# Optimization experiments

Hardware: AMD Instinct MI355X
Metric: run time of the kernel (lower is better)

The kernel has to match this reference:

```python
import jax, jax.numpy as jnp
import numpy as np

POOLED_SIZES = [12, 16, 20, 24]
NUM_HEADS = 8
EPS_LN = 1e-5


def _pool_mat(in_size, out_size):
    # torch adaptive_avg_pool1d/2d semantics as an averaging matrix [out, in]
    m = np.zeros((out_size, in_size), np.float32)
    for i in range(out_size):
        s = (i * in_size) // out_size
        e = -((-(i + 1) * in_size) // out_size)  # ceil
        m[i, s:e] = 1.0 / (e - s)
    return jnp.asarray(m)


def _dwconv(x, w, b):
    # depthwise 3x3, stride 1, padding 1 (NCHW, OIHW with I=1)
    y = jax.lax.conv_general_dilated(
        x, w, (1, 1), 'SAME', feature_group_count=x.shape[1],
        dimension_numbers=('NCHW', 'OIHW', 'NCHW'))
    return y + b[None, :, None, None]


def _ln(x, g, b):
    m = x.mean(-1, keepdims=True)
    v = jnp.mean((x - m) ** 2, axis=-1, keepdims=True)
    return (x - m) / jnp.sqrt(v + EPS_LN) * g + b


def setup_inputs() -> dict:
    key = jax.random.key(0)
    ks = jax.random.split(key, 16)
    B, H, W, C = 4, 56, 56, 256
    hid = 4 * C
    nrm = lambda k, shape, s=0.02: jax.random.normal(k, shape, jnp.float32) * s
    inp = {
        'x': jax.random.normal(ks[0], (B, H * W, C), jnp.float32),
        'cpe_w': nrm(ks[1], (C, 1, 3, 3)), 'cpe_b': jnp.zeros((C,), jnp.float32),
        'norm1_w': jnp.ones((C,), jnp.float32), 'norm1_b': jnp.zeros((C,), jnp.float32),
        'q_w': nrm(ks[2], (C, C)),
        'kv_w': nrm(ks[3], (2 * C, C)),
        'attn_norm_w': jnp.ones((C,), jnp.float32), 'attn_norm_b': jnp.zeros((C,), jnp.float32),
        'proj_w': nrm(ks[4], (C, C)), 'proj_b': jnp.zeros((C,), jnp.float32),
        'norm2_w': jnp.ones((C,), jnp.float32), 'norm2_b': jnp.zeros((C,), jnp.float32),
        'fc1_w': nrm(ks[5], (hid, C)), 'fc1_b': jnp.zeros((hid,), jnp.float32),
        'irb_conv_w': nrm(ks[6], (hid, 1, 3, 3)), 'irb_conv_b': jnp.zeros((hid,), jnp.float32),
        'fc2_w': nrm(ks[7], (C, hid)), 'fc2_b': jnp.zeros((C,), jnp.float32),
        'H': H, 'W': W,
    }
    for i in range(4):
        inp[f'dconv{i}_w'] = nrm(ks[8 + i], (C, 1, 3, 3))
        inp[f'dconv{i}_b'] = jnp.zeros((C,), jnp.float32)
    return inp


def _forward(x, cpe_w, cpe_b, norm1_w, norm1_b, q_w, kv_w, attn_norm_w, attn_norm_b,
             proj_w, proj_b, dconv0_w, dconv0_b, dconv1_w, dconv1_b, dconv2_w, dconv2_b,
             dconv3_w, dconv3_b, norm2_w, norm2_b, fc1_w, fc1_b, irb_conv_w, irb_conv_b,
             fc2_w, fc2_b, H, W):
    B, N, C = x.shape
    nh = NUM_HEADS
    hd = C // nh
    scale = hd ** -0.5
    # conditional positional encoding: x = cpe(x) + x
    xi = x.transpose(0, 2, 1).reshape(B, C, H, W)
    xi = _dwconv(xi, cpe_w, cpe_b) + xi
    x = xi.reshape(B, C, N).transpose(0, 2, 1)
    # ---- pyramid pooling attention ----
    xn = _ln(x, norm1_w, norm1_b)
    q = (xn @ q_w.T).reshape(B, N, nh, hd).transpose(0, 2, 1, 3)  # [B,nh,N,hd]
    x_ = xn.transpose(0, 2, 1).reshape(B, C, H, W)
    dws = [(dconv0_w, dconv0_b), (dconv1_w, dconv1_b),
           (dconv2_w, dconv2_b), (dconv3_w, dconv3_b)]
    pools = []
    for p, (dw, db) in zip(POOLED_SIZES, dws):
        ph = _pool_mat(H, p)
        pw = _pool_mat(W, p)
        pool = jnp.einsum('oi,bcij,pj->bcop', ph, x_, pw)  # adaptive avg pool (p,p)
        pool = pool + _dwconv(pool, dw, db)
        pools.append(pool.reshape(B, C, -1))
    pools = jnp.concatenate(pools, axis=2).transpose(0, 2, 1)  # [B,P,C], P=1376
    pools = _ln(pools, attn_norm_w, attn_norm_b)
    kv = (pools @ kv_w.T).reshape(B, -1, 2, nh, hd).transpose(2, 0, 3, 1, 4)
    k, v = kv[0], kv[1]  # [B,nh,P,hd]
    attn = jax.nn.softmax(jnp.einsum('bhnd,bhpd->bhnp', q, k) * scale, axis=-1)
    out = jnp.einsum('bhnp,bhpd->bhnd', attn, v).transpose(0, 2, 1, 3).reshape(B, N, C)
    out = out @ proj_w.T + proj_b
    x = x + out
    # ---- IRB FFN ----
    xn = _ln(x, norm2_w, norm2_b)
    xi = xn.transpose(0, 2, 1).reshape(B, C, H, W)
    h = jnp.einsum('oc,bchw->bohw', fc1_w, xi) + fc1_b[None, :, None, None]
    h = jax.nn.gelu(h, approximate=False)
    h = h + _dwconv(h, irb_conv_w, irb_conv_b)
    o = jnp.einsum('oc,bchw->bohw', fc2_w, h) + fc2_b[None, :, None, None]
    x = x + o.reshape(B, C, N).transpose(0, 2, 1)
    return x


def reference(x, cpe_w, cpe_b, norm1_w, norm1_b, q_w, kv_w, attn_norm_w, attn_norm_b,
              proj_w, proj_b, dconv0_w, dconv0_b, dconv1_w, dconv1_b, dconv2_w, dconv2_b,
              dconv3_w, dconv3_b, norm2_w, norm2_b, fc1_w, fc1_b, irb_conv_w, irb_conv_b,
              fc2_w, fc2_b, H, W):
    return _forward(x, cpe_w, cpe_b, norm1_w, norm1_b, q_w, kv_w, attn_norm_w, attn_norm_b,
                    proj_w, proj_b, dconv0_w, dconv0_b, dconv1_w, dconv1_b, dconv2_w, dconv2_b,
                    dconv3_w, dconv3_b, norm2_w, norm2_b, fc1_w, fc1_b, irb_conv_w, irb_conv_b,
                    fc2_w, fc2_b, H, W)
```

## Files before the change

kernel.cpp:

```cpp
#include <hip/hip_runtime.h>
#include <hip/hip_bf16.h>

#define BQ 4
#define HH 56
#define WW 56
#define NN (HH*WW)
#define CC 256
#define NHEAD 8
#define HD 32
#define PP 1376
#define PPAD 1408
#define HIDN 1024
#define EPS_LN 1e-5f
#define QSCALE_LOG2E 0.25503484f

typedef unsigned short bf16u;
typedef __attribute__((ext_vector_type(8))) short short8;
typedef __attribute__((ext_vector_type(4))) float f32x4;

__device__ __forceinline__ float bf2f(bf16u u){
  union { unsigned int i; float f; } v; v.i = ((unsigned int)u) << 16; return v.f;
}
__device__ __forceinline__ bf16u f2bf(float f){
  unsigned int x = __float_as_uint(f);
  x += 0x7fffu + ((x >> 16) & 1u);
  return (bf16u)(x >> 16);
}
__device__ __forceinline__ bf16u f2bf_r(float f){
  return (bf16u)((__float_as_uint(f) + 0x8000u) >> 16);
}
__device__ __forceinline__ void cvt4(const ushort4 u, float* d){
  d[0]=bf2f(u.x); d[1]=bf2f(u.y); d[2]=bf2f(u.z); d[3]=bf2f(u.w);
}

__device__ __forceinline__ void bar_lgkm(){
  asm volatile("s_waitcnt lgkmcnt(0)" ::: "memory");
  __builtin_amdgcn_s_barrier();
  asm volatile("" ::: "memory");
}

#define CSEG 4
__global__ void k_init(const float* __restrict__ qw, const float* __restrict__ kvw,
                       const float* __restrict__ pw, const float* __restrict__ f1,
                       const float* __restrict__ f2, bf16u* __restrict__ wo,
                       const float* __restrict__ x, const float* __restrict__ w,
                       const float* __restrict__ bias, const float* __restrict__ g,
                       const float* __restrict__ be, float* __restrict__ x1,
                       bf16u* __restrict__ xnb){
  if (blockIdx.x < 768){
    int off = (blockIdx.x*256 + threadIdx.x) * 4;
    const float* s;
    if (off < 65536)       s = qw  + off;
    else if (off < 196608) s = kvw + off - 65536;
    else if (off < 262144) s = pw  + off - 196608;
    else if (off < 524288) s = f1  + off - 262144;
    else                   s = f2  + off - 524288;
    float4 v = *(const float4*)s;
    ushort4 u = {f2bf(v.x), f2bf(v.y), f2bf(v.z), f2bf(v.w)};
    *(ushort4*)(wo + off) = u;
    return;
  }
  int t = threadIdx.x;
  int wave = t >> 6, lane = t & 63;
  int widx = (blockIdx.x - 768)*4 + wave;
  const int nseg = WW/CSEG;
  int xseg = widx % nseg;
  int y    = (widx / nseg) % HH;
  int b    = widx / (nseg*HH);
  int c0 = lane*4;
  int x0 = xseg*CSEG;
  float wv[36];
  {
    const float* wp = w + (size_t)c0*9;
#pragma unroll
    for (int i = 0; i < 9; i++){
      float4 v = *(const float4*)(wp + i*4);
      wv[i*4+0]=v.x; wv[i*4+1]=v.y; wv[i*4+2]=v.z; wv[i*4+3]=v.w;
    }
  }
  float4 bi4 = *(const float4*)&bias[c0];
  float bi[4] = {bi4.x, bi4.y, bi4.z, bi4.w};
  float4 gv = *(const float4*)&g[c0];
  float4 bv = *(const float4*)&be[c0];
  const float* rowc = x + ((size_t)b*NN + (size_t)y*WW)*CC + c0;
  const float* rowm = (y > 0)    ? rowc - (size_t)WW*CC : rowc;
  const float* rowp = (y < HH-1) ? rowc + (size_t)WW*CC : rowc;
  if (y == 0){
#pragma unroll
    for (int cc = 0; cc < 4; cc++){ wv[cc*9+0]=0.f; wv[cc*9+1]=0.f; wv[cc*9+2]=0.f; }
  }
  if (y == HH-1){
#pragma unroll
    for (int cc = 0; cc < 4; cc++){ wv[cc*9+6]=0.f; wv[cc*9+7]=0.f; wv[cc*9+8]=0.f; }
  }
  float win[3][3][4];
  float4 rawA[3], rawB[3];
  if (x0 == 0){
#pragma unroll
    for (int r = 0; r < 3; r++)
#pragma unroll
      for (int cc = 0; cc < 4; cc++) win[0][r][cc] = 0.f;
  } else {
    size_t o = (size_t)(x0-1)*CC;
    float4 a0 = *(const float4*)&rowm[o];
    float4 a1 = *(const float4*)&rowc[o];
    float4 a2 = *(const float4*)&rowp[o];
    win[0][0][0]=a0.x; win[0][0][1]=a0.y; win[0][0][2]=a0.z; win[0][0][3]=a0.w;
    win[0][1][0]=a1.x; win[0][1][1]=a1.y; win[0][1][2]=a1.z; win[0][1][3]=a1.w;
    win[0][2][0]=a2.x; win[0][2][1]=a2.y; win[0][2][2]=a2.z; win[0][2][3]=a2.w;
  }
  {
    size_t o = (size_t)x0*CC;
    float4 a0 = *(const float4*)&rowm[o];
    float4 a1 = *(const float4*)&rowc[o];
    float4 a2 = *(const float4*)&rowp[o];
    win[1][0][0]=a0.x; win[1][0][1]=a0.y; win[1][0][2]=a0.z; win[1][0][3]=a0.w;
    win[1][1][0]=a1.x; win[1][1][1]=a1.y; win[1][1][2]=a1.z; win[1][1][3]=a1.w;
    win[1][2][0]=a2.x; win[1][2][1]=a2.y; win[1][2][2]=a2.z; win[1][2][3]=a2.w;
  }
  {
    size_t o = (size_t)(x0+1)*CC;
    rawA[0] = *(const float4*)&rowm[o];
    rawA[1] = *(const float4*)&rowc[o];
    rawA[2] = *(const float4*)&rowp[o];
  }
#pragma unroll
  for (int xx = 0; xx < CSEG; xx++){
    float4* cur = (xx & 1) ? rawB : rawA;
    float4* nxt = (xx & 1) ? rawA : rawB;
    if (xx < CSEG-1){
      int xg = x0 + xx + 2;
      if (xg < WW){
        size_t o = (size_t)xg*CC;
        nxt[0] = *(const float4*)&rowm[o];
        nxt[1] = *(const float4*)&rowc[o];
        nxt[2] = *(const float4*)&rowp[o];
      } else {
        float4 z = {0.f,0.f,0.f,0.f};
        nxt[0] = z; nxt[1] = z; nxt[2] = z;
      }
    }
    int sl2 = (xx+2)%3, slm = xx%3, slc = (xx+1)%3;
#pragma unroll
    for (int r = 0; r < 3; r++){
      win[sl2][r][0]=cur[r].x; win[sl2][r][1]=cur[r].y;
      win[sl2][r][2]=cur[r].z; win[sl2][r][3]=cur[r].w;
    }
    float o4[4];
#pragma unroll
    for (int cc = 0; cc < 4; cc++){
      float a = bi[cc];
      a += win[slm][0][cc]*wv[cc*9+0] + win[slc][0][cc]*wv[cc*9+1] + win[sl2][0][cc]*wv[cc*9+2];
      a += win[slm][1][cc]*wv[cc*9+3] + win[slc][1][cc]*wv[cc*9+4] + win[sl2][1][cc]*wv[cc*9+5];
      a += win[slm][2][cc]*wv[cc*9+6] + win[slc][2][cc]*wv[cc*9+7] + win[sl2][2][cc]*wv[cc*9+8];
      o4[cc] = win[slc][1][cc] + a;
    }
    size_t pix = (size_t)b*NN + (size_t)y*WW + x0 + xx;
    float4 ov = {o4[0],o4[1],o4[2],o4[3]};
    *(float4*)&x1[pix*CC + c0] = ov;
    float s  = o4[0]+o4[1]+o4[2]+o4[3];
    float s2 = o4[0]*o4[0]+o4[1]*o4[1]+o4[2]*o4[2]+o4[3]*o4[3];
#pragma unroll
    for (int off = 32; off; off >>= 1){
      s  += __shfl_xor(s,  off);
      s2 += __shfl_xor(s2, off);
    }
    float mean = s * (1.f/CC);
    float var  = s2 * (1.f/CC) - mean*mean;
    float rstd = rsqrtf(var + EPS_LN);
    float y0 = (o4[0]-mean)*rstd*gv.x + bv.x;
    float y1 = (o4[1]-mean)*rstd*gv.y + bv.y;
    float y2 = (o4[2]-mean)*rstd*gv.z + bv.z;
    float y3 = (o4[3]-mean)*rstd*gv.w + bv.w;
    ushort4 yb = {f2bf_r(y0), f2bf_r(y1), f2bf_r(y2), f2bf_r(y3)};
    *(ushort4*)&xnb[pix*CC + c0] = yb;
  }
}

__global__ void k_ln_bf16(const float* __restrict__ X, const float* __restrict__ g,
                          const float* __restrict__ be, bf16u* __restrict__ Y){
  int wave = threadIdx.x >> 6, lane = threadIdx.x & 63;
  int row = blockIdx.x*4 + wave;
  int c0 = lane*4;
  float4 v = *(const float4*)&X[(size_t)row*CC + c0];
  float s  = v.x+v.y+v.z+v.w;
  float s2 = v.x*v.x+v.y*v.y+v.z*v.z+v.w*v.w;
#pragma unroll
  for (int off = 32; off; off >>= 1){
    s  += __shfl_xor(s,  off);
    s2 += __shfl_xor(s2, off);
  }
  float mean = s * (1.f/CC);
  float var  = s2 * (1.f/CC) - mean*mean;
  float rstd = rsqrtf(var + EPS_LN);
  float4 gv = *(const float4*)&g[c0];
  float4 bv = *(const float4*)&be[c0];
  ushort4 yb = {f2bf_r((v.x-mean)*rstd*gv.x + bv.x),
                f2bf_r((v.y-mean)*rstd*gv.y + bv.y),
                f2bf_r((v.z-mean)*rstd*gv.z + bv.z),
                f2bf_r((v.w-mean)*rstd*gv.w + bv.w)};
  *(ushort4*)&Y[(size_t)row*CC + c0] = yb;
}

#define GST 40
template<int MT, int NT, bool OUT_BF16, bool HAS_BIAS, bool DO_GELU, bool HAS_RES, bool VT_OUT>
__device__ __forceinline__ void gemm_body(int bx, int by,
                       const bf16u* __restrict__ A, const bf16u* __restrict__ Wt,
                       const float* __restrict__ bias, void* Outp,
                       const float* Res, bf16u* __restrict__ vtout,
                       int Nout, int K, float oscale,
                       bf16u* __restrict__ AshB, bf16u* __restrict__ BshB){
  constexpr int MW = (MT == 128) ? 4 : 2;
  constexpr int NW = (NT == 128) ? 4 : 2;
  bf16u* Ash0 = AshB; bf16u* Ash1 = AshB + MT*GST;
  bf16u* Bsh0 = BshB; bf16u* Bsh1 = BshB + NT*GST;
  int t = threadIdx.x;
  int wave = t >> 6, lane = t & 63, quad = lane >> 4, l16 = lane & 15;
  int m0 = by * MT, n0 = bx * NT;
  int wm = (wave >> 1) * (MT/2);
  int wn = (wave & 1) * (NT/2);
  int ar = (MT==128) ? (t>>1) : (t>>2);
  int ac = (MT==128) ? ((t&1)*16) : ((t&3)*8);
  int br = (NT==128) ? (t>>1) : (t>>2);
  int bc = (NT==128) ? ((t&1)*16) : ((t&3)*8);
  int astore = ar*GST + ac;
  int bstore = br*GST + bc;
  const bf16u* ap = A  + (size_t)(m0+ar)*K + ac;
  const bf16u* bp = Wt + (size_t)(n0+br)*K + bc;

  {
    uint4 t0 = *(const uint4*)ap;
    *(uint4*)&Ash0[astore] = t0;
    if constexpr (MT == 128){ uint4 t1 = *(const uint4*)(ap+8); *(uint4*)&Ash0[astore+8] = t1; }
    uint4 t2 = *(const uint4*)bp;
    *(uint4*)&Bsh0[bstore] = t2;
    if constexpr (NT == 128){ uint4 t3 = *(const uint4*)(bp+8); *(uint4*)&Bsh0[bstore+8] = t3; }
  }
  uint4 aA0, aA1, bA0, bA1;
  uint4 aB0, aB1, bB0, bB1;
  ap += 32; bp += 32;
  aA0 = *(const uint4*)ap;
  if constexpr (MT == 128) aA1 = *(const uint4*)(ap+8);
  bA0 = *(const uint4*)bp;
  if constexpr (NT == 128) bA1 = *(const uint4*)(bp+8);
  ap += 32; bp += 32;
  aB0 = *(const uint4*)ap;
  if constexpr (MT == 128) aB1 = *(const uint4*)(ap+8);
  bB0 = *(const uint4*)bp;
  if constexpr (NT == 128) bB1 = *(const uint4*)(bp+8);
  ap += 32; bp += 32;
  bar_lgkm();

  f32x4 zero = {0.f,0.f,0.f,0.f};
  f32x4 acc[MW][NW];
#pragma unroll
  for (int i = 0; i < MW; i++)
#pragma unroll
    for (int j = 0; j < NW; j++) acc[i][j] = zero;

  int nks = K >> 5;

#define GEMM_STEP(AshP, BshP) { \
    short8 af[MW], bfr[NW]; \
    _Pragma("unroll") \
    for (int mi = 0; mi < MW; mi++) \
      af[mi] = *(const short8*)&AshP[(wm + mi*16 + l16)*GST + quad*8]; \
    _Pragma("unroll") \
    for (int ni = 0; ni < NW; ni++) \
      bfr[ni] = *(const short8*)&BshP[(wn + ni*16 + l16)*GST + quad*8]; \
    _Pragma("unroll") \
    for (int mi = 0; mi < MW; mi++) \
      _Pragma("unroll") \
      for (int ni = 0; ni < NW; ni++) \
        acc[mi][ni] = __builtin_amdgcn_mfma_f32_16x16x32_bf16(af[mi], bfr[ni], acc[mi][ni], 0,0,0); }

  for (int ks = 0; ks < nks; ks += 2){
    if (ks < nks-1){
      *(uint4*)&Ash1[astore] = aA0;
      if constexpr (MT == 128) *(uint4*)&Ash1[astore+8] = aA1;
      *(uint4*)&Bsh1[bstore] = bA0;
      if constexpr (NT == 128) *(uint4*)&Bsh1[bstore+8] = bA1;
      if (ks < nks-3){
        aA0 = *(const uint4*)ap;
        if constexpr (MT == 128) aA1 = *(const uint4*)(ap+8);
        bA0 = *(const uint4*)bp;
        if constexpr (NT == 128) bA1 = *(const uint4*)(bp+8);
        ap += 32; bp += 32;
      }
    }
    GEMM_STEP(Ash0, Bsh0)
    if (ks < nks-1) bar_lgkm();
    if (ks+1 < nks-1){
      *(uint4*)&Ash0[astore] = aB0;
      if constexpr (MT == 128) *(uint4*)&Ash0[astore+8] = aB1;
      *(uint4*)&Bsh0[bstore] = bB0;
      if constexpr (NT == 128) *(uint4*)&Bsh0[bstore+8] = bB1;
      if (ks+1 < nks-3){
        aB0 = *(const uint4*)ap;
        if constexpr (MT == 128) aB1 = *(const uint4*)(ap+8);
        bB0 = *(const uint4*)bp;
        if constexpr (NT == 128) bB1 = *(const uint4*)(bp+8);
        ap += 32; bp += 32;
      }
    }
    if (ks+1 < nks){
      GEMM_STEP(Ash1, Bsh1)
      if (ks+1 < nks-1) bar_lgkm();
    }
  }
#undef GEMM_STEP

#pragma unroll
  for (int mi = 0; mi < MW; mi++){
#pragma unroll
    for (int r = 0; r < 4; r++){
      int row = m0 + wm + mi*16 + quad*4 + r;
#pragma unroll
      for (int ni = 0; ni < NW; ni++){
        int col = n0 + wn + ni*16 + l16;
        float v = acc[mi][ni][r] * oscale;
        if constexpr (HAS_BIAS) v += bias[col];
        if constexpr (DO_GELU)  v = 0.5f*v*(1.f + erff(v*0.70710678118654752f));
        if constexpr (HAS_RES)  v += Res[(size_t)row*Nout + col];
        if constexpr (VT_OUT){
          if (col < CC){
            ((bf16u*)Outp)[(size_t)row*Nout + col] = f2bf_r(v);
          } else {
            int bb = row / PP, pp = row - bb*PP;
            vtout[((size_t)(bb*CC + (col - CC)))*PPAD + pp] = f2bf_r(v);
          }
        } else if constexpr (OUT_BF16){
          ((bf16u*)Outp)[(size_t)row*Nout + col] = f2bf_r(v);
        } else {
          ((float*)Outp)[(size_t)row*Nout + col] = v;
        }
      }
    }
  }
}

template<int MT, int NT, bool OUT_BF16, bool HAS_BIAS, bool DO_GELU, bool HAS_RES, bool VT_OUT>
__global__ __launch_bounds__(256) void k_gemm_mfma(const bf16u* __restrict__ A,
                       const bf16u* __restrict__ Wt,
                       const float* __restrict__ bias, void* Outp,
                       const float* Res, bf16u* __restrict__ vtout,
                       int NX, int Nout, int K, float oscale){
  __shared__ bf16u Ash[2][MT*GST];
  __shared__ bf16u Bsh[2][NT*GST];
  int i = blockIdx.x;
  int w = (i & 7) * ((int)gridDim.x >> 3) + (i >> 3);
  int bx = w % NX, by = w / NX;
  gemm_body<MT,NT,OUT_BF16,HAS_BIAS,DO_GELU,HAS_RES,VT_OUT>(
      bx, by, A, Wt, bias, Outp, Res, vtout, Nout, K, oscale,
      &Ash[0][0], &Bsh[0][0]);
}

#define QGRID ((CC/64)*(BQ*NN/64))
__global__ __launch_bounds__(256) void k_qpool(const bf16u* __restrict__ xnb,
                       const bf16u* __restrict__ wq, bf16u* __restrict__ qb,
                       float* __restrict__ praw){
  __shared__ bf16u Ash[2][64*GST];
  __shared__ bf16u Bsh[2][64*GST];
  if (blockIdx.x < QGRID){
    int i = blockIdx.x;
    int w = (i & 7) * (QGRID >> 3) + (i >> 3);
    int bx = w & 3, by = w >> 2;
    gemm_body<64,64,true,false,false,false,false>(
        bx, by, xnb, wq, nullptr, qb, nullptr, nullptr, CC, CC, QSCALE_LOG2E,
        &Ash[0][0], &Bsh[0][0]);
    return;
  }
  int wave = threadIdx.x >> 6, lane = threadIdx.x & 63;
  int bp = (blockIdx.x - QGRID)*4 + wave;
  int b = bp / PP, p = bp % PP;
  int ps, pi;
  if (p < 144)      { ps = 12; pi = p; }
  else if (p < 400) { ps = 16; pi = p - 144; }
  else if (p < 800) { ps = 20; pi = p - 400; }
  else              { ps = 24; pi = p - 800; }
  int oi = pi / ps, oj = pi % ps;
  int si = oi*HH/ps, ei = ((oi+1)*HH + ps - 1)/ps;
  int sj = oj*WW/ps, ej = ((oj+1)*WW + ps - 1)/ps;
  int c0 = lane*4;
  const bf16u* xb = xnb + (size_t)b*NN*CC + c0;
  float a0=0.f, a1=0.f, a2=0.f, a3=0.f;
  for (int i = si; i < ei; i++)
    for (int j = sj; j < ej; j++){
      ushort4 v = *(const ushort4*)&xb[(size_t)(i*WW+j)*CC];
      a0 += bf2f(v.x); a1 += bf2f(v.y); a2 += bf2f(v.z); a3 += bf2f(v.w);
    }
  float inv = 1.f / (float)((ei-si)*(ej-sj));
  float4 o = {a0*inv, a1*inv, a2*inv, a3*inv};
  *(float4*)&praw[(size_t)bp*CC + c0] = o;
}

__global__ void k_pooldw_ln(const float* __restrict__ praw,
    const float* w0, const float* b0, const float* w1, const float* b1,
    const float* w2, const float* b2, const float* w3, const float* b3,
    const float* __restrict__ g, const float* __restrict__ be,
    bf16u* __restrict__ pools){
  int bp = blockIdx.x;
  int b = bp / PP, p = bp % PP;
  int ps, pi, off; const float *w, *bi;
  if (p < 144)      { ps=12; pi=p;     off=0;   w=w0; bi=b0; }
  else if (p < 400) { ps=16; pi=p-144; off=144; w=w1; bi=b1; }
  else if (p < 800) { ps=20; pi=p-400; off=400; w=w2; bi=b2; }
  else              { ps=24; pi=p-800; off=800; w=w3; bi=b3; }
  int oi = pi/ps, oj = pi%ps;
  int c = threadIdx.x;
  const float* base = praw + (size_t)(b*PP + off)*CC + c;
  float acc = bi[c];
#pragma unroll
  for (int kh = 0; kh < 3; kh++){
    int ii = oi + kh - 1; if (ii < 0 || ii >= ps) continue;
#pragma unroll
    for (int kw = 0; kw < 3; kw++){
      int jj = oj + kw - 1; if (jj < 0 || jj >= ps) continue;
      acc += base[(size_t)(ii*ps+jj)*CC] * w[c*9 + kh*3 + kw];
    }
  }
  float v = base[(size_t)(oi*ps+oj)*CC] + acc;
  float s = v, s2 = v*v;
#pragma unroll
  for (int o2_ = 32; o2_; o2_ >>= 1){
    s  += __shfl_down(s,  o2_);
    s2 += __shfl_down(s2, o2_);
  }
  __shared__ float red[10];
  int wv_ = c >> 6, ln = c & 63;
  if (ln == 0){ red[wv_] = s; red[4+wv_] = s2; }
  __syncthreads();
  if (c == 0){
    float S  = red[0]+red[1]+red[2]+red[3];
    float S2 = red[4]+red[5]+red[6]+red[7];
    float mean = S * (1.f/CC);
    float var  = S2 * (1.f/CC) - mean*mean;
    red[8] = mean; red[9] = rsqrtf(var + EPS_LN);
  }
  __syncthreads();
  float mean = red[8], rstd = red[9];
  pools[(size_t)bp*CC + c] = f2bf_r((v - mean) * rstd * g[c] + be[c]);
}

#define KST 40
#define VST 72
__global__ __launch_bounds__(256) void k_attn_mfma(const bf16u* __restrict__ q,
                       const bf16u* __restrict__ kvb, const bf16u* __restrict__ vt,
                       bf16u* __restrict__ out){
  __shared__ bf16u Ksh[2][64*KST];
  __shared__ bf16u Vsh[2][32*VST];
  int t = threadIdx.x;
  int wave = t >> 6, lane = t & 63, quad = lane >> 4, l16 = lane & 15;
  int i = blockIdx.x;
  int bid = (i & 7) * 196 + (i >> 3);
  int qt = bid % (NN/64);
  int h  = (bid / (NN/64)) % NHEAD;
  int b  = bid / ((NN/64)*NHEAD);
  int q0 = qt*64 + wave*16;
  const bf16u* qptr = q + (size_t)(b*NN + q0 + l16)*CC + h*HD + quad*8;
  short8 qf = *(const short8*)qptr;
  f32x4 zero = {0.f,0.f,0.f,0.f};
  f32x4 o0 = zero, o1 = zero, osum = zero;
  const short8 onesf = {0x3F80,0x3F80,0x3F80,0x3F80,0x3F80,0x3F80,0x3F80,0x3F80};
  int ksr = t >> 2, ksc = (t & 3) * 8;
  int vsr = t >> 3, vsc = (t & 7) * 8;
  const bf16u* ksrc = kvb + (size_t)(b*PP + ksr)*(2*CC) + h*HD + ksc;
  const bf16u* vsrc = vt  + (size_t)(b*CC + h*HD + vsr)*PPAD + vsc;
  int krow = (ksr & 32) | ((ksr & 4) << 2) | ((ksr & 24) >> 1) | (ksr & 3);
  int kstore = krow*KST + ksc;
  int vstore = vsr*VST + vsc;
  int koffA = l16*KST + quad*8;
  int koffB = koffA + 16*KST;
  int voff0 = l16*VST + quad*8;
  int voff1 = (16 + l16)*VST + quad*8;

  uint4 kreg = *(const uint4*)ksrc;
  uint4 vreg = *(const uint4*)vsrc;
  *(uint4*)&Ksh[0][kstore] = kreg;
  *(uint4*)&Vsh[0][vstore] = vreg;
  ksrc += (size_t)64*(2*CC); vsrc += 64;
  kreg = *(const uint4*)ksrc; vreg = *(const uint4*)vsrc;
  bar_lgkm();

#define PAIR(KB, VB, cb) { \
    short8 kfa = *(const short8*)&KB[cb*KST + koffA]; \
    short8 kfb = *(const short8*)&KB[cb*KST + koffB]; \
    f32x4 sa = __builtin_amdgcn_mfma_f32_16x16x32_bf16(kfa, qf, zero, 0,0,0); \
    f32x4 sb = __builtin_amdgcn_mfma_f32_16x16x32_bf16(kfb, qf, zero, 0,0,0); \
    float ea0 = __builtin_amdgcn_exp2f(sa[0]), ea1 = __builtin_amdgcn_exp2f(sa[1]); \
    float ea2 = __builtin_amdgcn_exp2f(sa[2]), ea3 = __builtin_amdgcn_exp2f(sa[3]); \
    float eb0 = __builtin_amdgcn_exp2f(sb[0]), eb1 = __builtin_amdgcn_exp2f(sb[1]); \
    float eb2 = __builtin_amdgcn_exp2f(sb[2]), eb3 = __builtin_amdgcn_exp2f(sb[3]); \
    unsigned ra0 = __float_as_uint(ea0) + 0x8000u, ra1 = __float_as_uint(ea1) + 0x8000u; \
    unsigned ra2 = __float_as_uint(ea2) + 0x8000u, ra3 = __float_as_uint(ea3) + 0x8000u; \
    unsigned rb0 = __float_as_uint(eb0) + 0x8000u, rb1 = __float_as_uint(eb1) + 0x8000u; \
    unsigned rb2 = __float_as_uint(eb2) + 0x8000u, rb3 = __float_as_uint(eb3) + 0x8000u; \
    union { uint4 u; short8 s; } pk; \
    pk.u.x = __builtin_amdgcn_perm(ra1, ra0, 0x07060302u); \
    pk.u.y = __builtin_amdgcn_perm(ra3, ra2, 0x07060302u); \
    pk.u.z = __builtin_amdgcn_perm(rb1, rb0, 0x07060302u); \
    pk.u.w = __builtin_amdgcn_perm(rb3, rb2, 0x07060302u); \
    short8 pa = pk.s; \
    short8 vf0 = *(const short8*)&VB[cb + voff0]; \
    short8 vf1 = *(const short8*)&VB[cb + voff1]; \
    o0 = __builtin_amdgcn_mfma_f32_16x16x32_bf16(pa, vf0, o0, 0,0,0); \
    o1 = __builtin_amdgcn_mfma_f32_16x16x32_bf16(pa, vf1, o1, 0,0,0); \
    osum = __builtin_amdgcn_mfma_f32_16x16x32_bf16(pa, onesf, osum, 0,0,0); }

  for (int ch = 0; ch < PPAD/64 - 1; ch++){
    int cur = ch & 1;
    bf16u* KB = &Ksh[cur][0];
    bf16u* VB = &Vsh[cur][0];
    *(uint4*)&Ksh[cur^1][kstore] = kreg;
    *(uint4*)&Vsh[cur^1][vstore] = vreg;
    if (ch < PPAD/64 - 2){
      ksrc += (size_t)64*(2*CC); vsrc += 64;
      kreg = *(const uint4*)ksrc; vreg = *(const uint4*)vsrc;
    }
    PAIR(KB, VB, 0)
    PAIR(KB, VB, 32)
    bar_lgkm();
  }
  {
    bf16u* KB = &Ksh[1][0];
    bf16u* VB = &Vsh[1][0];
    PAIR(KB, VB, 0)
  }
#undef PAIR

#pragma unroll
  for (int r = 0; r < 4; r++){
    int qq = quad*4 + r;
    float inv = 1.f / osum[r];
    size_t base = (size_t)(b*NN + q0 + qq)*CC + h*HD;
    out[base + l16]      = f2bf_r(o0[r]*inv);
    out[base + 16 + l16] = f2bf_r(o1[r]*inv);
  }
}

#define DWSEG 8
__global__ __launch_bounds__(256) void k_dwh(const bf16u* __restrict__ h, const float* __restrict__ w,
                      const float* __restrict__ bias, bf16u* __restrict__ h2){
  const int nseg = WW/DWSEG;
  int bid = blockIdx.x;
  int xseg = bid % nseg;
  int y    = (bid / nseg) % HH;
  int b    = bid / (nseg*HH);
  int t = threadIdx.x;
  int c0 = t*4;
  int x0 = xseg*DWSEG;
  float wv[36];
  {
    const float4* wp = (const float4*)(w + (size_t)c0*9);
#pragma unroll
    for (int i = 0; i < 9; i++){
      float4 v = wp[i];
      wv[i*4+0]=v.x; wv[i*4+1]=v.y; wv[i*4+2]=v.z; wv[i*4+3]=v.w;
    }
  }
  float4 bi4 = *(const float4*)&bias[c0];
  float bi[4] = {bi4.x, bi4.y, bi4.z, bi4.w};
  const bf16u* rowc = h + ((size_t)b*NN + (size_t)y*WW)*HIDN + c0;
  const bf16u* rowm = (y > 0)    ? rowc - (size_t)WW*HIDN : rowc;
  const bf16u* rowp = (y < HH-1) ? rowc + (size_t)WW*HIDN : rowc;
  if (y == 0){
#pragma unroll
    for (int cc = 0; cc < 4; cc++){ wv[cc*9+0]=0.f; wv[cc*9+1]=0.f; wv[cc*9+2]=0.f; }
  }
  if (y == HH-1){
#pragma unroll
    for (int cc = 0; cc < 4; cc++){ wv[cc*9+6]=0.f; wv[cc*9+7]=0.f; wv[cc*9+8]=0.f; }
  }
  float win[3][3][4];
  ushort4 rawA[3], rawB[3];
  if (x0 == 0){
#pragma unroll
    for (int r = 0; r < 3; r++)
#pragma unroll
      for (int cc = 0; cc < 4; cc++) win[0][r][cc] = 0.f;
  } else {
    size_t o = (size_t)(x0-1)*HIDN;
    ushort4 a0 = *(const ushort4*)&rowm[o];
    ushort4 a1 = *(const ushort4*)&rowc[o];
    ushort4 a2 = *(const ushort4*)&rowp[o];
    cvt4(a0, win[0][0]); cvt4(a1, win[0][1]); cvt4(a2, win[0][2]);
  }
  {
    size_t o = (size_t)x0*HIDN;
    ushort4 a0 = *(const ushort4*)&rowm[o];
    ushort4 a1 = *(const ushort4*)&rowc[o];
    ushort4 a2 = *(const ushort4*)&rowp[o];
    cvt4(a0, win[1][0]); cvt4(a1, win[1][1]); cvt4(a2, win[1][2]);
  }
  {
    size_t o = (size_t)(x0+1)*HIDN;
    rawA[0] = *(const ushort4*)&rowm[o];
    rawA[1] = *(const ushort4*)&rowc[o];
    rawA[2] = *(const ushort4*)&rowp[o];
  }
#pragma unroll
  for (int x = 0; x < DWSEG; x++){
    ushort4* cur = (x & 1) ? rawB : rawA;
    ushort4* nxt = (x & 1) ? rawA : rawB;
    if (x < DWSEG-1){
      int xg = x0 + x + 2;
      if (xg < WW){
        size_t o = (size_t)xg*HIDN;
        nxt[0] = *(const ushort4*)&rowm[o];
        nxt[1] = *(const ushort4*)&rowc[o];
        nxt[2] = *(const ushort4*)&rowp[o];
      } else {
        ushort4 z = {0,0,0,0};
        nxt[0] = z; nxt[1] = z; nxt[2] = z;
      }
    }
    int s2 = (x+2)%3, sm = x%3, sc_ = (x+1)%3;
    cvt4(cur[0], win[s2][0]); cvt4(cur[1], win[s2][1]); cvt4(cur[2], win[s2][2]);
    float o0[4];
#pragma unroll
    for (int cc = 0; cc < 4; cc++){
      float a = bi[cc];
      a += win[sm][0][cc]*wv[cc*9+0] + win[sc_][0][cc]*wv[cc*9+1] + win[s2][0][cc]*wv[cc*9+2];
      a += win[sm][1][cc]*wv[cc*9+3] + win[sc_][1][cc]*wv[cc*9+4] + win[s2][1][cc]*wv[cc*9+5];
      a += win[sm][2][cc]*wv[cc*9+6] + win[sc_][2][cc]*wv[cc*9+7] + win[s2][2][cc]*wv[cc*9+8];
      o0[cc] = win[sc_][1][cc] + a;
    }
    ushort4 ou = {f2bf_r(o0[0]), f2bf_r(o0[1]), f2bf_r(o0[2]), f2bf_r(o0[3])};
    *(ushort4*)&h2[((size_t)b*NN + (size_t)y*WW + x0 + x)*HIDN + c0] = ou;
  }
}

extern "C" void kernel_launch(void* const* d_in, const int* in_sizes, int n_in,
                              void* d_out, int out_size, void* d_ws, size_t ws_size,
                              hipStream_t stream){
  const float* x      = (const float*)d_in[0];
  const float* cpe_w  = (const float*)d_in[1];
  const float* cpe_b  = (const float*)d_in[2];
  const float* n1w    = (const float*)d_in[3];
  const float* n1b    = (const float*)d_in[4];
  const float* q_w    = (const float*)d_in[5];
  const float* kv_w   = (const float*)d_in[6];
  const float* anw    = (const float*)d_in[7];
  const float* anb    = (const float*)d_in[8];
  const float* proj_w = (const float*)d_in[9];
  const float* proj_b = (const float*)d_in[10];
  const float* n2w    = (const float*)d_in[11];
  const float* n2b    = (const float*)d_in[12];
  const float* fc1_w  = (const float*)d_in[13];
  const float* fc1_b  = (const float*)d_in[14];
  const float* irb_w  = (const float*)d_in[15];
  const float* irb_b  = (const float*)d_in[16];
  const float* fc2_w  = (const float*)d_in[17];
  const float* fc2_b  = (const float*)d_in[18];
  const float* dw0    = (const float*)d_in[21];
  const float* db0    = (const float*)d_in[22];
  const float* dw1    = (const float*)d_in[23];
  const float* db1    = (const float*)d_in[24];
  const float* dw2    = (const float*)d_in[25];
  const float* db2    = (const float*)d_in[26];
  const float* dw3    = (const float*)d_in[27];
  const float* db3    = (const float*)d_in[28];

  const size_t BNC = (size_t)BQ*NN*CC;
  const size_t BPC = (size_t)BQ*PP*CC;
  const size_t BNH = (size_t)BQ*NN*HIDN;

  float* x1   = (float*)d_ws;
  bf16u* xnb  = (bf16u*)(x1 + BNC);
  bf16u* wbuf = xnb + BNC;
  bf16u* wq   = wbuf;
  bf16u* wkv  = wbuf + 65536;
  bf16u* wpj  = wbuf + 196608;
  bf16u* wf1  = wbuf + 262144;
  bf16u* wf2  = wbuf + 524288;
  float* A0   = (float*)(wbuf + 786432);
  bf16u* qb   = (bf16u*)A0;
  float* praw = (float*)(qb + BNC);
  bf16u* poolsb = (bf16u*)(praw + BPC);
  bf16u* kvb  = poolsb + BPC;
  bf16u* vtb  = kvb + (size_t)BQ*PP*2*CC;
  bf16u* hbuf = (bf16u*)A0;
  bf16u* h2buf = hbuf + BNH;

  k_init<<<768 + (BQ*HH*(WW/CSEG))/4, 256, 0, stream>>>(q_w, kv_w, proj_w, fc1_w, fc2_w, wbuf,
                                            x, cpe_w, cpe_b, n1w, n1b, x1, xnb);
  k_qpool<<<QGRID + BQ*PP/4, 256, 0, stream>>>(xnb, wq, qb, praw);
  k_pooldw_ln<<<BQ*PP, 256, 0, stream>>>(praw, dw0,db0, dw1,db1, dw2,db2, dw3,db3,
                                         anw, anb, poolsb);
  k_gemm_mfma<64,64,true,false,false,false,true><<<(2*CC/64)*(BQ*PP/64), 256, 0, stream>>>(
      poolsb, wkv, nullptr, kvb, nullptr, vtb, 2*CC/64, 2*CC, CC, 1.0f);
  k_attn_mfma<<<BQ*NHEAD*(NN/64), 256, 0, stream>>>(qb, kvb, vtb, qb);
  k_gemm_mfma<64,64,false,true,false,true,false><<<(CC/64)*(BQ*NN/64), 256, 0, stream>>>(
      qb, wpj, proj_b, x1, x1, nullptr, CC/64, CC, CC, 1.0f);
  k_ln_bf16<<<BQ*NN/4, 256, 0, stream>>>(x1, n2w, n2b, xnb);
  k_gemm_mfma<128,128,true,true,true,false,false><<<(HIDN/128)*(BQ*NN/128), 256, 0, stream>>>(
      xnb, wf1, fc1_b, hbuf, nullptr, nullptr, HIDN/128, HIDN, CC, 1.0f);
  k_dwh<<<BQ*HH*(WW/DWSEG), 256, 0, stream>>>(hbuf, irb_w, irb_b, h2buf);
  k_gemm_mfma<64,64,false,true,false,true,false><<<(CC/64)*(BQ*NN/64), 256, 0, stream>>>(
      h2buf, wf2, fc2_b, d_out, x1, nullptr, CC/64, CC, HIDN, 1.0f);
}
```

Baseline: 296.2 us.

## Deepen attention K/V prefetch to two chunks and shrink fc1 GEMM tile

The attention kernel's K/V streaming loop is unrolled by two with explicit ping-pong shared buffers. Global loads now run two chunks ahead using two register sets, so memory latency has more time to hide behind the MFMA and exp work. Separately, the fc1 GEMM tile changes from 128x128 to 64x128, doubling the block count for better occupancy and load balance. The cost is more live registers in attention and less data reuse per fc1 block.

```diff
diff --git a/kernel.cpp b/kernel.cpp
--- a/kernel.cpp
+++ b/kernel.cpp
@@ -466,6 +466,7 @@
   int vsr = t >> 3, vsc = (t & 7) * 8;
   const bf16u* ksrc = kvb + (size_t)(b*PP + ksr)*(2*CC) + h*HD + ksc;
   const bf16u* vsrc = vt  + (size_t)(b*CC + h*HD + vsr)*PPAD + vsc;
+  const size_t KSTEP = (size_t)64*(2*CC);
   int krow = (ksr & 32) | ((ksr & 4) << 2) | ((ksr & 24) >> 1) | (ksr & 3);
   int kstore = krow*KST + ksc;
   int vstore = vsr*VST + vsc;
@@ -473,18 +474,26 @@
   int koffB = koffA + 16*KST;
   int voff0 = l16*VST + quad*8;
   int voff1 = (16 + l16)*VST + quad*8;
-
-  uint4 kreg = *(const uint4*)ksrc;
-  uint4 vreg = *(const uint4*)vsrc;
-  *(uint4*)&Ksh[0][kstore] = kreg;
-  *(uint4*)&Vsh[0][vstore] = vreg;
-  ksrc += (size_t)64*(2*CC); vsrc += 64;
-  kreg = *(const uint4*)ksrc; vreg = *(const uint4*)vsrc;
+  bf16u* Ksh0 = &Ksh[0][0]; bf16u* Ksh1 = &Ksh[1][0];
+  bf16u* Vsh0 = &Vsh[0][0]; bf16u* Vsh1 = &Vsh[1][0];
+
+  {
+    uint4 k0 = *(const uint4*)ksrc;
+    uint4 v0 = *(const uint4*)vsrc;
+    *(uint4*)&Ksh0[kstore] = k0;
+    *(uint4*)&Vsh0[vstore] = v0;
+  }
+  uint4 kA, vA, kB, vB;
+  ksrc += KSTEP; vsrc += 64;
+  kA = *(const uint4*)ksrc; vA = *(const uint4*)vsrc;
+  ksrc += KSTEP; vsrc += 64;
+  kB = *(const uint4*)ksrc; vB = *(const uint4*)vsrc;
+  ksrc += KSTEP; vsrc += 64;
   bar_lgkm();
 
-#define PAIR(KB, VB, cb) { \
-    short8 kfa = *(const short8*)&KB[cb*KST + koffA]; \
-    short8 kfb = *(const short8*)&KB[cb*KST + koffB]; \
+#define PAIR(KB_, VB_, cb) { \
+    short8 kfa = *(const short8*)&KB_[cb*KST + koffA]; \
+    short8 kfb = *(const short8*)&KB_[cb*KST + koffB]; \
     f32x4 sa = __builtin_amdgcn_mfma_f32_16x16x32_bf16(kfa, qf, zero, 0,0,0); \
     f32x4 sb = __builtin_amdgcn_mfma_f32_16x16x32_bf16(kfb, qf, zero, 0,0,0); \
     float ea0 = __builtin_amdgcn_exp2f(sa[0]), ea1 = __builtin_amdgcn_exp2f(sa[1]); \
@@ -501,31 +510,36 @@
     pk.u.z = __builtin_amdgcn_perm(rb1, rb0, 0x07060302u); \
     pk.u.w = __builtin_amdgcn_perm(rb3, rb2, 0x07060302u); \
     short8 pa = pk.s; \
-    short8 vf0 = *(const short8*)&VB[cb + voff0]; \
-    short8 vf1 = *(const short8*)&VB[cb + voff1]; \
+    short8 vf0 = *(const short8*)&VB_[cb + voff0]; \
+    short8 vf1 = *(const short8*)&VB_[cb + voff1]; \
     o0 = __builtin_amdgcn_mfma_f32_16x16x32_bf16(pa, vf0, o0, 0,0,0); \
     o1 = __builtin_amdgcn_mfma_f32_16x16x32_bf16(pa, vf1, o1, 0,0,0); \
     osum = __builtin_amdgcn_mfma_f32_16x16x32_bf16(pa, onesf, osum, 0,0,0); }
 
-  for (int ch = 0; ch < PPAD/64 - 1; ch++){
-    int cur = ch & 1;
-    bf16u* KB = &Ksh[cur][0];
-    bf16u* VB = &Vsh[cur][0];
-    *(uint4*)&Ksh[cur^1][kstore] = kreg;
-    *(uint4*)&Vsh[cur^1][vstore] = vreg;
-    if (ch < PPAD/64 - 2){
-      ksrc += (size_t)64*(2*CC); vsrc += 64;
-      kreg = *(const uint4*)ksrc; vreg = *(const uint4*)vsrc;
-    }
-    PAIR(KB, VB, 0)
-    PAIR(KB, VB, 32)
+  for (int ch = 0; ch < 20; ch += 2){
+    *(uint4*)&Ksh1[kstore] = kA;
+    *(uint4*)&Vsh1[vstore] = vA;
+    kA = *(const uint4*)ksrc; vA = *(const uint4*)vsrc;
+    ksrc += KSTEP; vsrc += 64;
+    PAIR(Ksh0, Vsh0, 0)
+    PAIR(Ksh0, Vsh0, 32)
     bar_lgkm();
-  }
-  {
-    bf16u* KB = &Ksh[1][0];
-    bf16u* VB = &Vsh[1][0];
-    PAIR(KB, VB, 0)
-  }
+    *(uint4*)&Ksh0[kstore] = kB;
+    *(uint4*)&Vsh0[vstore] = vB;
+    if (ch+1 <= 17){
+      kB = *(const uint4*)ksrc; vB = *(const uint4*)vsrc;
+      ksrc += KSTEP; vsrc += 64;
+    }
+    PAIR(Ksh1, Vsh1, 0)
+    PAIR(Ksh1, Vsh1, 32)
+    bar_lgkm();
+  }
+  *(uint4*)&Ksh1[kstore] = kA;
+  *(uint4*)&Vsh1[vstore] = vA;
+  PAIR(Ksh0, Vsh0, 0)
+  PAIR(Ksh0, Vsh0, 32)
+  bar_lgkm();
+  PAIR(Ksh1, Vsh1, 0)
 #undef PAIR
 
 #pragma unroll
@@ -693,7 +707,7 @@
   k_gemm_mfma<64,64,false,true,false,true,false><<<(CC/64)*(BQ*NN/64), 256, 0, stream>>>(
       qb, wpj, proj_b, x1, x1, nullptr, CC/64, CC, CC, 1.0f);
   k_ln_bf16<<<BQ*NN/4, 256, 0, stream>>>(x1, n2w, n2b, xnb);
-  k_gemm_mfma<128,128,true,true,true,false,false><<<(HIDN/128)*(BQ*NN/128), 256, 0, stream>>>(
+  k_gemm_mfma<64,128,true,true,true,false,false><<<(HIDN/128)*(BQ*NN/64), 256, 0, stream>>>(
       xnb, wf1, fc1_b, hbuf, nullptr, nullptr, HIDN/128, HIDN, CC, 1.0f);
   k_dwh<<<BQ*HH*(WW/DWSEG), 256, 0, stream>>>(hbuf, irb_w, irb_b, h2buf);
   k_gemm_mfma<64,64,false,true,false,true,false><<<(CC/64)*(BQ*NN/64), 256, 0, stream>>>(
```

New measurement: 290.8 us. About the same (-1.8%).
